# Performance work log

Hardware: AMD Instinct MI355X
Metric: run time of the kernel (lower is better)

Reference implementation:

```python
import jax, jax.numpy as jnp
import numpy as np

RATE = 22050.0 / 256.0  # audio_target_rate from the torch source
SIZES = [2.23147392 * RATE, 2.62519274 * RATE, 3.74199546 * RATE,
         5.78800454 * RATE, 8.02371882 * RATE, float('inf')]
WEIGHT = 1.0
EPS = 1e-7


def _giou_1d(a, b):
    # a, b: [P, 2] intervals (start, end); elementwise 1-D GIoU
    inter = jnp.clip(jnp.minimum(a[:, 1], b[:, 1]) - jnp.maximum(a[:, 0], b[:, 0]), 0.0)
    union = (a[:, 1] - a[:, 0]) + (b[:, 1] - b[:, 0]) - inter
    iou = inter / (union + EPS)
    enclose = jnp.maximum(a[:, 1], b[:, 1]) - jnp.minimum(a[:, 0], b[:, 0])
    return iou - (enclose - union) / (enclose + EPS)


def setup_inputs() -> dict:
    key = jax.random.key(0)
    ks = jax.random.split(key, 4)
    B, N = 4, 32
    L0 = 131072  # frames at the finest level
    levels = 6
    anchors = {f"anchors_l{i}": (jnp.arange(L0 >> i, dtype=jnp.float32) + 0.5) * (2.0 ** i)
               for i in range(levels)}
    A = sum(int(v.shape[0]) for v in anchors.values())  # 258048
    # GT intervals: all rows belong to class 0 (matches class_id filter in the source)
    starts = jax.random.uniform(ks[0], (B, N), minval=0.0, maxval=float(L0) - 2000.0)
    lens = jax.random.uniform(ks[1], (B, N), minval=50.0, maxval=1500.0)
    annotations = jnp.stack([starts, starts + lens, jnp.zeros((B, N))], axis=-1).astype(jnp.float32)
    # Predicted intervals for every anchor
    c = jax.random.uniform(ks[2], (B, A), minval=0.0, maxval=float(L0))
    w = jax.random.uniform(ks[3], (B, A), minval=10.0, maxval=2000.0)
    regressions = jnp.stack([c - 0.5 * w, c + 0.5 * w], axis=-1).astype(jnp.float32)
    out = {"regressions": regressions, "annotations": annotations, "class_id": 0}
    out.update(anchors)
    return out


def reference(regressions, annotations, anchors_l0, anchors_l1, anchors_l2,
              anchors_l3, anchors_l4, anchors_l5, class_id):
    anchors_list = [anchors_l0, anchors_l1, anchors_l2, anchors_l3, anchors_l4, anchors_l5]
    all_pts = jnp.concatenate(anchors_list)  # [A]

    def per_sample(reg, ann):
        # ann: [N, 3]; inputs guarantee every row has class == class_id and is valid
        order = jnp.argsort(ann[:, 1] - ann[:, 0])  # sort GT by length ascending
        ann = ann[order]
        s, e = ann[:, 0:1], ann[:, 1:2]  # [N,1]
        pos_parts, nl_parts, nr_parts = [], [], []
        for i, pts in enumerate(anchors_list):
            l = pts[None, :] - s            # [N, A_i]
            r = e - pts[None, :]            # [N, A_i]
            in_gt = (l >= 0.0) & (r >= 0.0)
            m = jnp.maximum(l, r)
            lower = SIZES[i - 1] if i > 0 else 0.0
            cand = in_gt & (m >= lower) & (m < SIZES[i])
            pos_parts.append(cand.any(axis=0))
            amax = jnp.argmax(cand, axis=0)  # first True per anchor (0 if none)
            inv = 1.0 / (2.0 ** i)           # normalize l*/r* by 2**level
            nl_parts.append(jnp.take_along_axis(l, amax[None, :], axis=0)[0] * inv)
            nr_parts.append(jnp.take_along_axis(r, amax[None, :], axis=0)[0] * inv)
        pos = jnp.concatenate(pos_parts)   # [A] bool
        nl = jnp.concatenate(nl_parts)     # [A]
        nr = jnp.concatenate(nr_parts)     # [A]
        # decoded normalized target boxes around the anchor points
        boxes = jnp.stack([all_pts - nl, all_pts + nr], axis=1)  # [A, 2]
        giou = jnp.clip(_giou_1d(boxes, reg[:, :2]), -1.0, 1.0)
        loss = 1.0 - giou
        posf = pos.astype(loss.dtype)
        # masked mean over positive anchors (torch indexes by boolean mask then .mean())
        return jnp.sum(loss * posf) / jnp.maximum(jnp.sum(posf), 1.0) * WEIGHT

    return jax.vmap(per_sample)(regressions, annotations)  # [B] per-sample losses
```

## Files before the change

### kernel.cpp

```cpp
#include <hip/hip_runtime.h>

#define EPS_F 1e-7f
#define NN 32
#define MARGIN 3
#define NSEG (NN * 6)
#define TPB 512
#define CAND_MAX 10240

__global__ __launch_bounds__(TPB) void rl_fused(
    const float* __restrict__ reg,
    const float* __restrict__ ann,
    int c0, int A,
    float* __restrict__ out)
{
    const int b = blockIdx.x;
    const int t = threadIdx.x;
    const int wave = t >> 6;
    const int lane = t & 63;

    __shared__ float2 sh_se[NN];
    __shared__ int4   seg[NSEG];
    __shared__ int    pfx[NSEG];
    __shared__ unsigned char cand[CAND_MAX];
    __shared__ float  sh_sz[8];
    __shared__ float  red_l[TPB / 64], red_p[TPB / 64];

    if (t < 8) {
        const float szc[8] = {
            0.0f,
            (float)(2.23147392 * (22050.0 / 256.0)),
            (float)(2.62519274 * (22050.0 / 256.0)),
            (float)(3.74199546 * (22050.0 / 256.0)),
            (float)(5.78800454 * (22050.0 / 256.0)),
            (float)(8.02371882 * (22050.0 / 256.0)),
            __builtin_inff(), __builtin_inff()
        };
        sh_sz[t] = szc[t];
    }

    if (t < NN) {
        const float* an = ann + (size_t)b * (size_t)NN * 3;
        const float s0 = an[t * 3 + 0];
        const float e0 = an[t * 3 + 1];
        const float len = e0 - s0;
        int rank = 0;
#pragma unroll
        for (int j = 0; j < NN; ++j) {
            const float lj = __shfl(len, j, 64);
            rank += (lj < len) || (lj == len && j < t);
        }
        sh_se[rank] = make_float2(s0, e0);
    }
    __syncthreads();

    float sreg[NN], ereg[NN];
#pragma unroll
    for (int i = 0; i < NN; ++i) {
        const float2 se = sh_se[i];
        sreg[i] = se.x;
        ereg[i] = se.y;
    }

    if (t < NSEG) {
        const int n   = t / 6;
        const int lvl = t - n * 6;
        const float2 se = sh_se[n];
        const float s = se.x, e = se.y;
        const float mid   = 0.5f * (s + e);
        const float halfL = 0.5f * (e - s);
        const float lo = sh_sz[lvl];
        const float hi = sh_sz[lvl + 1];
        const int   cnt = c0 >> lvl;
        const float inv = __int_as_float((127 - lvl) << 23);

        const float dlo = fmaxf(lo - halfL, 0.0f);
        const float dhi = hi - halfL;
        const float prl = fmaxf(mid + dlo, s);
        const float prh = fminf(mid + dhi, e);
        const float pll = fmaxf(mid - dhi, s);
        const float plh = fminf(mid - dlo, e);

        int r0 = (int)floorf(prl * inv - 0.5f) - MARGIN;
        int r1 = (int)floorf(prh * inv - 0.5f) + MARGIN;
        int l0 = (int)floorf(pll * inv - 0.5f) - MARGIN;
        int l1 = (int)floorf(plh * inv - 0.5f) + MARGIN;
        r0 = max(r0, 0); r1 = min(r1, cnt - 1);
        l0 = max(l0, 0); l1 = min(l1, cnt - 1);
        if (r1 >= r0) l1 = min(l1, r0 - 1);
        const int lenL = max(l1 - l0 + 1, 0);
        const int lenR = max(r1 - r0 + 1, 0);
        seg[t] = make_int4(l0, r0, lenL | (lenR << 16), (n << 8) | lvl);
        pfx[t] = lenL + lenR;
    }
    __syncthreads();

#pragma unroll
    for (int off = 1; off < NSEG; off <<= 1) {
        int add = 0;
        if (t < NSEG && t >= off) add = pfx[t - off];
        __syncthreads();
        if (t < NSEG) pfx[t] += add;
        __syncthreads();
    }
    const int T = min(pfx[NSEG - 1], CAND_MAX);

    if (t < NSEG) {
        const int4 sg = seg[t];
        const int count = (sg.z & 0xffff) + (sg.z >> 16);
        const int start = pfx[t] - count;
        seg[t].w = sg.w | (start << 16);
        const int end = min(start + count, CAND_MAX);
        for (int i = start; i < end; ++i) cand[i] = (unsigned char)t;
    }
    __syncthreads();

    const int twoc0 = 2 * c0;
    float loss_sum = 0.0f, pos_sum = 0.0f;

    for (int j = t; j < T; j += TPB) {
        const int sid = cand[j];
        const int4 sg = seg[sid];
        const int lenL  = sg.z & 0xffff;
        const int start = sg.w >> 16;
        const int n     = (sg.w >> 8) & 0xff;
        const int lvl   = sg.w & 0xff;
        const int local = j - start;
        const int loc = (local < lenL) ? (sg.x + local) : (sg.y + (local - lenL));
        const float scale = __int_as_float((127 + lvl) << 23);
        const float inv   = __int_as_float((127 - lvl) << 23);
        const int aoff = twoc0 - (twoc0 >> lvl);

        const float2 g = ((const float2*)reg)[(size_t)b * A + (aoff + loc)];

        const float pt = ((float)loc + 0.5f) * scale;
        const float lo = sh_sz[lvl];
        const float hi = sh_sz[lvl + 1];
        const float s = sreg[0], e0_ = ereg[0];
        (void)s; (void)e0_;

        const float2 se = sh_se[n];
        const float l = pt - se.x;
        const float r = se.y - pt;
        const float m = fmaxf(l, r);
        bool valid = (fminf(l, r) >= 0.0f) & (m >= lo) & (m < hi);

        bool taken = false;
#pragma unroll
        for (int n2 = 0; n2 < NN - 1; ++n2) {
            const float l2 = pt - sreg[n2];
            const float r2 = ereg[n2] - pt;
            const float m2 = fmaxf(l2, r2);
            taken |= (n2 < n) & (fminf(l2, r2) >= 0.0f) & (m2 >= lo) & (m2 < hi);
        }
        valid = valid && !taken;

        const float b0 = pt - l * inv;
        const float b1 = pt + r * inv;
        const float inter = fmaxf(fminf(b1, g.y) - fmaxf(b0, g.x), 0.0f);
        const float uni = (b1 - b0) + (g.y - g.x) - inter;
        const float iou = inter * __builtin_amdgcn_rcpf(uni + EPS_F);
        const float enc = fmaxf(b1, g.y) - fminf(b0, g.x);
        float giou = iou - (enc - uni) * __builtin_amdgcn_rcpf(enc + EPS_F);
        giou = fminf(fmaxf(giou, -1.0f), 1.0f);
        loss_sum += valid ? (1.0f - giou) : 0.0f;
        pos_sum  += valid ? 1.0f : 0.0f;
    }

    for (int o = 32; o > 0; o >>= 1) {
        loss_sum += __shfl_down(loss_sum, o, 64);
        pos_sum  += __shfl_down(pos_sum,  o, 64);
    }
    if (lane == 0) { red_l[wave] = loss_sum; red_p[wave] = pos_sum; }
    __syncthreads();
    if (t == 0) {
        float Ls = 0.0f, Ps = 0.0f;
#pragma unroll
        for (int w = 0; w < TPB / 64; ++w) { Ls += red_l[w]; Ps += red_p[w]; }
        out[b] = Ls / fmaxf(Ps, 1.0f);
    }
}

extern "C" void kernel_launch(void* const* d_in, const int* in_sizes, int n_in,
                              void* d_out, int out_size, void* d_ws, size_t ws_size,
                              hipStream_t stream) {
    const float* reg = (const float*)d_in[0];
    const float* ann = (const float*)d_in[1];
    const int c0 = in_sizes[3];
    const int A = in_sizes[3] + in_sizes[4] + in_sizes[5] +
                  in_sizes[6] + in_sizes[7] + in_sizes[8];
    const int B = out_size;
    (void)d_ws; (void)ws_size;

    rl_fused<<<dim3(B), TPB, 0, stream>>>(reg, ann, c0, A, (float*)d_out);
}
```

Baseline: 84.45 us.

## Precompute per-segment overlap masks and double block size for candidate scan

```diff
diff --git a/kernel.cpp b/kernel.cpp
--- a/kernel.cpp
+++ b/kernel.cpp
@@ -4,8 +4,8 @@
 #define NN 32
 #define MARGIN 3
 #define NSEG (NN * 6)
-#define TPB 512
-#define CAND_MAX 10240
+#define TPB 1024
+#define CAND_MAX 24576
 
 __global__ __launch_bounds__(TPB) void rl_fused(
     const float* __restrict__ reg,
@@ -21,7 +21,8 @@
     __shared__ float2 sh_se[NN];
     __shared__ int4   seg[NSEG];
     __shared__ int    pfx[NSEG];
-    __shared__ unsigned char cand[CAND_MAX];
+    __shared__ unsigned segmask[NSEG];
+    __shared__ unsigned cand32[CAND_MAX / 4];
     __shared__ float  sh_sz[8];
     __shared__ float  red_l[TPB / 64], red_p[TPB / 64];
 
@@ -53,14 +54,6 @@
     }
     __syncthreads();
 
-    float sreg[NN], ereg[NN];
-#pragma unroll
-    for (int i = 0; i < NN; ++i) {
-        const float2 se = sh_se[i];
-        sreg[i] = se.x;
-        ereg[i] = se.y;
-    }
-
     if (t < NSEG) {
         const int n   = t / 6;
         const int lvl = t - n * 6;
@@ -71,7 +64,8 @@
         const float lo = sh_sz[lvl];
         const float hi = sh_sz[lvl + 1];
         const int   cnt = c0 >> lvl;
-        const float inv = __int_as_float((127 - lvl) << 23);
+        const float inv   = __int_as_float((127 - lvl) << 23);
+        const float scale = __int_as_float((127 + lvl) << 23);
 
         const float dlo = fmaxf(lo - halfL, 0.0f);
         const float dhi = hi - halfL;
@@ -91,17 +85,35 @@
         const int lenR = max(r1 - r0 + 1, 0);
         seg[t] = make_int4(l0, r0, lenL | (lenR << 16), (n << 8) | lvl);
         pfx[t] = lenL + lenR;
-    }
-    __syncthreads();
-
-#pragma unroll
-    for (int off = 1; off < NSEG; off <<= 1) {
-        int add = 0;
-        if (t < NSEG && t >= off) add = pfx[t - off];
-        __syncthreads();
-        if (t < NSEG) pfx[t] += add;
-        __syncthreads();
-    }
+
+        const int firstloc = lenL ? l0 : r0;
+        const int lastloc  = lenR ? r1 : l1;
+        const float ptmin = ((float)firstloc + 0.5f) * scale;
+        const float ptmax = ((float)lastloc  + 0.5f) * scale;
+        unsigned msk = 0u;
+        for (int n2 = 0; n2 < n; ++n2) {
+            const float2 o = sh_se[n2];
+            if ((o.x <= ptmax) & (o.y >= ptmin)) msk |= (1u << n2);
+        }
+        segmask[t] = msk;
+    }
+    __syncthreads();
+
+    if (wave == 0) {
+        int carry = 0;
+#pragma unroll
+        for (int k = 0; k < 3; ++k) {
+            int v = pfx[k * 64 + lane];
+#pragma unroll
+            for (int o = 1; o < 64; o <<= 1) {
+                const int u = __shfl_up(v, o, 64);
+                v += (lane >= o) ? u : 0;
+            }
+            pfx[k * 64 + lane] = v + carry;
+            carry += __shfl(v, 63, 64);
+        }
+    }
+    __syncthreads();
     const int T = min(pfx[NSEG - 1], CAND_MAX);
 
     if (t < NSEG) {
@@ -109,19 +121,26 @@
         const int count = (sg.z & 0xffff) + (sg.z >> 16);
         const int start = pfx[t] - count;
         seg[t].w = sg.w | (start << 16);
+        unsigned char* cb = (unsigned char*)cand32;
+        int i = start;
         const int end = min(start + count, CAND_MAX);
-        for (int i = start; i < end; ++i) cand[i] = (unsigned char)t;
+        const unsigned rep = 0x01010101u * (unsigned)t;
+        while (i < end && (i & 3)) cb[i++] = (unsigned char)t;
+        for (; i + 4 <= end; i += 4) cand32[i >> 2] = rep;
+        for (; i < end; ++i) cb[i] = (unsigned char)t;
     }
     __syncthreads();
 
     const int twoc0 = 2 * c0;
+    const unsigned char* cb = (const unsigned char*)cand32;
     float loss_sum = 0.0f, pos_sum = 0.0f;
 
     for (int j = t; j < T; j += TPB) {
-        const int sid = cand[j];
+        const int sid = cb[j];
         const int4 sg = seg[sid];
+        unsigned msk = segmask[sid];
         const int lenL  = sg.z & 0xffff;
-        const int start = sg.w >> 16;
+        const int start = (int)(((unsigned)sg.w) >> 16);
         const int n     = (sg.w >> 8) & 0xff;
         const int lvl   = sg.w & 0xff;
         const int local = j - start;
@@ -135,24 +154,21 @@
         const float pt = ((float)loc + 0.5f) * scale;
         const float lo = sh_sz[lvl];
         const float hi = sh_sz[lvl + 1];
-        const float s = sreg[0], e0_ = ereg[0];
-        (void)s; (void)e0_;
-
         const float2 se = sh_se[n];
         const float l = pt - se.x;
         const float r = se.y - pt;
         const float m = fmaxf(l, r);
         bool valid = (fminf(l, r) >= 0.0f) & (m >= lo) & (m < hi);
 
-        bool taken = false;
-#pragma unroll
-        for (int n2 = 0; n2 < NN - 1; ++n2) {
-            const float l2 = pt - sreg[n2];
-            const float r2 = ereg[n2] - pt;
+        while (valid && msk) {
+            const int n2 = __builtin_ctz(msk);
+            msk &= msk - 1u;
+            const float2 o = sh_se[n2];
+            const float l2 = pt - o.x;
+            const float r2 = o.y - pt;
             const float m2 = fmaxf(l2, r2);
-            taken |= (n2 < n) & (fminf(l2, r2) >= 0.0f) & (m2 >= lo) & (m2 < hi);
-        }
-        valid = valid && !taken;
+            if ((fminf(l2, r2) >= 0.0f) & (m2 >= lo) & (m2 < hi)) valid = false;
+        }
 
         const float b0 = pt - l * inv;
         const float b1 = pt + r * inv;
@@ -172,11 +188,15 @@
     }
     if (lane == 0) { red_l[wave] = loss_sum; red_p[wave] = pos_sum; }
     __syncthreads();
-    if (t == 0) {
-        float Ls = 0.0f, Ps = 0.0f;
-#pragma unroll
-        for (int w = 0; w < TPB / 64; ++w) { Ls += red_l[w]; Ps += red_p[w]; }
-        out[b] = Ls / fmaxf(Ps, 1.0f);
+    if (t < 16) {
+        float Ls = red_l[t];
+        float Ps = red_p[t];
+#pragma unroll
+        for (int o = 8; o > 0; o >>= 1) {
+            Ls += __shfl_down(Ls, o, 16);
+            Ps += __shfl_down(Ps, o, 16);
+        }
+        if (t == 0) out[b] = Ls / fmaxf(Ps, 1.0f);
     }
 }
 
```

Measured after the change: 76.48 us. -9.4%, faster.
